# Kernel tuning notes

Measured on AMD Instinct MI355X. Metric: run time of the kernel, lower is better.

## Reference

```python
import jax, jax.numpy as jnp
import numpy as np

NEG_SLOPE = 0.2
BN_EPS = 1e-5


def gat_conv(x, src, dst, num_nodes, W, att_src, att_dst, bias, concat):
    # x: [N, F_in]; W: [F_in, H*C]; att_src/att_dst: [H, C]
    H, C = att_src.shape
    h = (x @ W).reshape(num_nodes, H, C)                 # [N, H, C]
    a_src = jnp.einsum('nhc,hc->nh', h, att_src)          # [N, H]
    a_dst = jnp.einsum('nhc,hc->nh', h, att_dst)          # [N, H]
    e = a_src[src] + a_dst[dst]                           # [E, H]
    e = jax.nn.leaky_relu(e, NEG_SLOPE)
    # segment softmax over edges sharing the same destination node
    m = jax.ops.segment_max(e, dst, num_segments=num_nodes)   # [N, H]
    ex = jnp.exp(e - m[dst])
    denom = jax.ops.segment_sum(ex, dst, num_segments=num_nodes)  # [N, H]
    alpha = ex / (denom[dst] + 1e-16)                     # [E, H]
    msg = h[src] * alpha[:, :, None]                      # [E, H, C]
    out = jax.ops.segment_sum(msg, dst, num_segments=num_nodes)   # [N, H, C]
    if concat:
        return out.reshape(num_nodes, H * C) + bias
    return out.mean(axis=1) + bias


def batch_norm(x, gamma, beta):
    mu = x.mean(axis=0)
    var = x.var(axis=0)
    return (x - mu) * jax.lax.rsqrt(var + BN_EPS) * gamma + beta


def setup_inputs() -> dict:
    key = jax.random.key(0)
    ks = jax.random.split(key, 16)
    N, E, F_in, C, H, NC = 50000, 800000, 128, 16, 8, 2
    s = lambda k, shape, fan: jax.random.normal(k, shape, jnp.float32) * (1.0 / np.sqrt(fan))
    inp = {
        'x': jax.random.normal(ks[0], (N, F_in), jnp.float32),
        'edge_index': jax.random.randint(ks[1], (2, E), 0, N, jnp.int32),
        'W0': s(ks[2], (F_in, H * C), F_in),
        'att_src0': s(ks[3], (H, C), C),
        'att_dst0': s(ks[4], (H, C), C),
        'b0': jnp.zeros((H * C,), jnp.float32),
        'gamma0': jnp.ones((H * C,), jnp.float32),
        'beta0': jnp.zeros((H * C,), jnp.float32),
        'W1': s(ks[5], (H * C, H * C), H * C),
        'att_src1': s(ks[6], (H, C), C),
        'att_dst1': s(ks[7], (H, C), C),
        'b1': jnp.zeros((C,), jnp.float32),
        'gamma1': jnp.ones((C,), jnp.float32),
        'beta1': jnp.zeros((C,), jnp.float32),
        'Wc': s(ks[8], (C, NC), C),
        'bc': jnp.zeros((NC,), jnp.float32),
    }
    return inp


def reference(x, edge_index, W0, att_src0, att_dst0, b0, gamma0, beta0,
              W1, att_src1, att_dst1, b1, gamma1, beta1, Wc, bc):
    N = x.shape[0]
    loop = jnp.arange(N, dtype=edge_index.dtype)
    src = jnp.concatenate([edge_index[0], loop])  # add self-loops (PyG default)
    dst = jnp.concatenate([edge_index[1], loop])
    # layer 0: concat heads -> [N, H*C]
    h = gat_conv(x, src, dst, N, W0, att_src0, att_dst0, b0, concat=True)
    h = batch_norm(h, gamma0, beta0)
    h = jax.nn.elu(h)
    # layer 1: average heads -> [N, C]
    h = gat_conv(h, src, dst, N, W1, att_src1, att_dst1, b1, concat=False)
    h = batch_norm(h, gamma1, beta1)
    logits = h @ Wc + bc
    return logits
```

## Files before the change

kernel.cpp:

```cpp
#include <hip/hip_runtime.h>
#include <math.h>

#define NEG_SLOPE 0.2f
#define BN_EPS 1e-5f


__device__ __forceinline__ void edge_sd(const int* __restrict__ ei, int E, int eid, int& s, int& d) {
    if (eid < E) { s = ei[eid]; d = ei[E + eid]; }
    else         { s = d = eid - E; }
}

__device__ __forceinline__ float lrelu(float v) { return v > 0.f ? v : NEG_SLOPE * v; }

__device__ __forceinline__ unsigned short f2bf(float f) {
    unsigned u = __float_as_uint(f);
    u += 0x7fffu + ((u >> 16) & 1u);
    return (unsigned short)(u >> 16);
}

__global__ __launch_bounds__(256) void gemm128(const float* __restrict__ X,
                                               const float* __restrict__ W,
                                               float* __restrict__ Y,
                                               unsigned short* __restrict__ Ybf,
                                               const float* __restrict__ bnmu,
                                               const float* __restrict__ bnrs,
                                               const float* __restrict__ gamma,
                                               const float* __restrict__ beta,
                                               int Nrows) {
    __shared__ float xs[64 * 128];
    int bm = blockIdx.x * 64;
    int tid = threadIdx.x;

    const float4* Xv = (const float4*)(X + (size_t)bm * 128);
    float4* xsv = (float4*)xs;
    if (bnmu == nullptr) {
        for (int i = tid; i < 64 * 32; i += 256) {
            int row = i >> 5;
            xsv[i] = (bm + row < Nrows) ? Xv[i] : make_float4(0.f, 0.f, 0.f, 0.f);
        }
    } else {
        for (int i = tid; i < 64 * 32; i += 256) {
            int row = i >> 5;
            int cb = (i & 31) * 4;
            float4 v = (bm + row < Nrows) ? Xv[i] : make_float4(0.f, 0.f, 0.f, 0.f);
            float4 m4 = *(const float4*)(bnmu + cb);
            float4 r4 = *(const float4*)(bnrs + cb);
            float4 g4 = *(const float4*)(gamma + cb);
            float4 b4 = *(const float4*)(beta + cb);
            v.x = (v.x - m4.x) * r4.x * g4.x + b4.x;
            v.y = (v.y - m4.y) * r4.y * g4.y + b4.y;
            v.z = (v.z - m4.z) * r4.z * g4.z + b4.z;
            v.w = (v.w - m4.w) * r4.w * g4.w + b4.w;
            v.x = v.x > 0.f ? v.x : expm1f(v.x);
            v.y = v.y > 0.f ? v.y : expm1f(v.y);
            v.z = v.z > 0.f ? v.z : expm1f(v.z);
            v.w = v.w > 0.f ? v.w : expm1f(v.w);
            xsv[i] = v;
        }
    }
    __syncthreads();

    int cq = tid & 31;
    int rg = tid >> 5;

    float acc[8][4];
#pragma unroll
    for (int r = 0; r < 8; r++)
#pragma unroll
        for (int j = 0; j < 4; j++) acc[r][j] = 0.f;

    const float* xbase = xs + (rg * 8) * 128;
#pragma unroll 4
    for (int k = 0; k < 128; k++) {
        float4 w4 = *(const float4*)(W + k * 128 + cq * 4);
#pragma unroll
        for (int r = 0; r < 8; r++) {
            float xv = xbase[r * 128 + k];
            acc[r][0] += xv * w4.x;
            acc[r][1] += xv * w4.y;
            acc[r][2] += xv * w4.z;
            acc[r][3] += xv * w4.w;
        }
    }
#pragma unroll
    for (int r = 0; r < 8; r++) {
        int row = bm + rg * 8 + r;
        if (row < Nrows) {
            *(float4*)(Y + (size_t)row * 128 + cq * 4) =
                make_float4(acc[r][0], acc[r][1], acc[r][2], acc[r][3]);
            ushort4 pk;
            pk.x = f2bf(acc[r][0]);
            pk.y = f2bf(acc[r][1]);
            pk.z = f2bf(acc[r][2]);
            pk.w = f2bf(acc[r][3]);
            *(ushort4*)(Ybf + (size_t)row * 128 + cq * 4) = pk;
        }
    }
}

__global__ void att_kernel(const float* __restrict__ Hm,
                           const float* __restrict__ att_s,
                           const float* __restrict__ att_d,
                           float* __restrict__ a_src, float* __restrict__ a_dst, int N) {
    int idx = blockIdx.x * 256 + threadIdx.x;
    if (idx >= N * 8) return;
    int n = idx >> 3, h = idx & 7;
    const float* hp = Hm + (size_t)n * 128 + h * 16;
    float ss = 0.f, sd = 0.f;
#pragma unroll
    for (int c = 0; c < 16; c++) {
        float v = hp[c];
        ss += v * att_s[h * 16 + c];
        sd += v * att_d[h * 16 + c];
    }
    a_src[idx] = ss;
    a_dst[idx] = sd;
}

__global__ void hist_kernel(const int* __restrict__ ei, int E, int Etot,
                            int* __restrict__ counts, int* __restrict__ rank) {
    int eid = blockIdx.x * 256 + threadIdx.x;
    if (eid >= Etot) return;
    int s, d;
    edge_sd(ei, E, eid, s, d);
    rank[eid] = atomicAdd(&counts[d], 1);
}

__global__ __launch_bounds__(256) void chunksum_kernel(const int* __restrict__ counts,
                                                       int* __restrict__ csum, int N) {
    __shared__ int red[256];
    int base = blockIdx.x * 1024;
    int s = 0;
    for (int i = threadIdx.x; i < 1024; i += 256) {
        int idx = base + i;
        s += (idx < N) ? counts[idx] : 0;
    }
    red[threadIdx.x] = s;
    __syncthreads();
#pragma unroll
    for (int st = 128; st > 0; st >>= 1) {
        if (threadIdx.x < st) red[threadIdx.x] += red[threadIdx.x + st];
        __syncthreads();
    }
    if (threadIdx.x == 0) csum[blockIdx.x] = red[0];
}

__global__ void chunkscan_kernel(int* __restrict__ csum, int nchunk) {
    int lane = threadIdx.x;
    int v = (lane < nchunk) ? csum[lane] : 0;
    int incl = v;
#pragma unroll
    for (int off = 1; off < 64; off <<= 1) {
        int t = __shfl_up(incl, off);
        if (lane >= off) incl += t;
    }
    if (lane < nchunk) csum[lane] = incl - v;
}

__global__ __launch_bounds__(1024) void scanfinal_kernel(const int* __restrict__ counts,
                                                         const int* __restrict__ csum,
                                                         int* __restrict__ rowptr, int N) {
    __shared__ int wsum[16], woff_s[16];
    int tid = threadIdx.x, lane = tid & 63, wid = tid >> 6;
    int idx = blockIdx.x * 1024 + tid;
    int v = (idx < N) ? counts[idx] : 0;
    int incl = v;
#pragma unroll
    for (int off = 1; off < 64; off <<= 1) {
        int t = __shfl_up(incl, off);
        if (lane >= off) incl += t;
    }
    if (lane == 63) wsum[wid] = incl;
    __syncthreads();
    if (wid == 0 && lane < 16) {
        int w = wsum[lane], iw = w;
#pragma unroll
        for (int off = 1; off < 16; off <<= 1) {
            int t = __shfl_up(iw, off);
            if (lane >= off) iw += t;
        }
        woff_s[lane] = iw - w;
    }
    __syncthreads();
    if (idx < N) rowptr[idx + 1] = csum[blockIdx.x] + woff_s[wid] + incl;
    if (blockIdx.x == 0 && tid == 0) rowptr[0] = 0;
}

__global__ void scatter_kernel(const int* __restrict__ ei, int E, int Etot,
                               const int* __restrict__ rowptr, const int* __restrict__ rank,
                               unsigned short* __restrict__ ssrc) {
    int eid = blockIdx.x * 256 + threadIdx.x;
    if (eid >= Etot) return;
    int s, d;
    edge_sd(ei, E, eid, s, d);
    ssrc[rowptr[d] + rank[eid]] = (unsigned short)s;
}

template <bool MEAN>
__global__ __launch_bounds__(256) void agg_kernel(const int* __restrict__ rowptr,
                                                  const unsigned short* __restrict__ ssrc,
                                                  const float* __restrict__ a_src,
                                                  const float* __restrict__ a_dst,
                                                  const unsigned short* __restrict__ Hbf,
                                                  float* __restrict__ outbuf, int N) {
    int wid = threadIdx.x >> 6;
    int dst = blockIdx.x * 4 + wid;
    if (dst >= N) return;
    int lane = threadIdx.x & 63;
    int j  = lane >> 3;
    int hj = lane & 7;
    int hf = lane >> 3;
    int f  = lane * 2;
    int start = rowptr[dst], end = rowptr[dst + 1];
    float adst = a_dst[dst * 8 + hj];

    float acc0 = 0.f, acc1 = 0.f, denl = 0.f;
    for (int base = start; base < end; base += 8) {
        int i = base + j;
        int s = (i < end) ? (int)ssrc[i] : -1;
        float w = 0.f;
        if (s >= 0) w = __expf(lrelu(a_src[s * 8 + hj] + adst));
        denl += w;

        int   sA[8];
        float wA[8];
        unsigned uA[8];
#pragma unroll
        for (int j2 = 0; j2 < 8; j2++) {
            sA[j2] = __shfl(s, j2 * 8);
            wA[j2] = __shfl(w, j2 * 8 + hf);
        }
#pragma unroll
        for (int j2 = 0; j2 < 8; j2++)
            uA[j2] = (sA[j2] >= 0) ? *(const unsigned*)(Hbf + (size_t)sA[j2] * 128 + f) : 0u;
#pragma unroll
        for (int j2 = 0; j2 < 8; j2++) {
            acc0 += wA[j2] * __uint_as_float(uA[j2] << 16);
            acc1 += wA[j2] * __uint_as_float(uA[j2] & 0xffff0000u);
        }
    }
#pragma unroll
    for (int off = 8; off < 64; off <<= 1) denl += __shfl_xor(denl, off);
    float den = __shfl(denl, hf);
    float inv = 1.f / (den + 1e-16f);
    if (!MEAN) {
        *(float2*)(outbuf + (size_t)dst * 128 + f) = make_float2(acc0 * inv, acc1 * inv);
    } else {
        float r0 = acc0 * inv, r1 = acc1 * inv;
#pragma unroll
        for (int off = 8; off < 64; off <<= 1) {
            r0 += __shfl_xor(r0, off);
            r1 += __shfl_xor(r1, off);
        }
        if (lane < 8)
            *(float2*)(outbuf + (size_t)dst * 16 + lane * 2) =
                make_float2(r0 * 0.125f, r1 * 0.125f);
    }
}

template <int C>
__global__ __launch_bounds__(256) void stats_part_kernel(const float* __restrict__ X, int Nrows,
                                                         float* __restrict__ partial,
                                                         int rows_per_block) {
    constexpr int GSZ = 256 / C;
    __shared__ float ls[256], lq[256];
    int c = threadIdx.x % C;
    int g = threadIdx.x / C;
    long base = (long)blockIdx.x * rows_per_block;
    long endr = base + rows_per_block;
    if (endr > Nrows) endr = Nrows;
    float s = 0.f, q = 0.f;
    for (long r = base + g; r < endr; r += GSZ) {
        float v = X[r * C + c];
        s += v;
        q += v * v;
    }
    ls[threadIdx.x] = s;
    lq[threadIdx.x] = q;
    __syncthreads();
#pragma unroll
    for (int st = GSZ / 2; st > 0; st >>= 1) {
        if (g < st) {
            ls[threadIdx.x] += ls[threadIdx.x + st * C];
            lq[threadIdx.x] += lq[threadIdx.x + st * C];
        }
        __syncthreads();
    }
    if (g == 0) {
        partial[(size_t)blockIdx.x * (2 * C) + c] = ls[c];
        partial[(size_t)blockIdx.x * (2 * C) + C + c] = lq[c];
    }
}

template <int C>
__global__ __launch_bounds__(1024) void stats_final_kernel(const float* __restrict__ partial,
                                                           int nblk, float invN,
                                                           float* __restrict__ mu,
                                                           float* __restrict__ rsig) {
    constexpr int G = 1024 / C;
    __shared__ float ls[1024], lq[1024];
    int c = threadIdx.x % C;
    int g = threadIdx.x / C;
    float s = 0.f, q = 0.f;
    for (int b = g; b < nblk; b += G) {
        s += partial[(size_t)b * (2 * C) + c];
        q += partial[(size_t)b * (2 * C) + C + c];
    }
    ls[threadIdx.x] = s;
    lq[threadIdx.x] = q;
    __syncthreads();
#pragma unroll
    for (int st = G / 2; st > 0; st >>= 1) {
        if (g < st) {
            ls[threadIdx.x] += ls[threadIdx.x + st * C];
            lq[threadIdx.x] += lq[threadIdx.x + st * C];
        }
        __syncthreads();
    }
    if (g == 0) {
        float m_ = ls[c] * invN;
        float v = lq[c] * invN - m_ * m_;
        mu[c] = m_;
        rsig[c] = rsqrtf(v + BN_EPS);
    }
}

__global__ void final_kernel(const float* __restrict__ out1,
                             const float* __restrict__ mu, const float* __restrict__ rsig,
                             const float* __restrict__ gamma, const float* __restrict__ beta,
                             const float* __restrict__ Wc, const float* __restrict__ bc,
                             float* __restrict__ out, int N) {
    int n = blockIdx.x * 256 + threadIdx.x;
    if (n >= N) return;
    float l0 = bc[0], l1 = bc[1];
#pragma unroll
    for (int c = 0; c < 16; c++) {
        float v = (out1[(size_t)n * 16 + c] - mu[c]) * rsig[c] * gamma[c] + beta[c];
        l0 += v * Wc[c * 2 + 0];
        l1 += v * Wc[c * 2 + 1];
    }
    out[(size_t)n * 2 + 0] = l0;
    out[(size_t)n * 2 + 1] = l1;
}

extern "C" void kernel_launch(void* const* d_in, const int* in_sizes, int n_in,
                              void* d_out, int out_size, void* d_ws, size_t ws_size,
                              hipStream_t stream) {
    const float* x   = (const float*)d_in[0];
    const int*   ei  = (const int*)d_in[1];
    const float* W0  = (const float*)d_in[2];
    const float* as0 = (const float*)d_in[3];
    const float* ad0 = (const float*)d_in[4];
    const float* g0  = (const float*)d_in[6];
    const float* be0 = (const float*)d_in[7];
    const float* W1  = (const float*)d_in[8];
    const float* as1 = (const float*)d_in[9];
    const float* ad1 = (const float*)d_in[10];
    const float* g1  = (const float*)d_in[12];
    const float* be1 = (const float*)d_in[13];
    const float* Wc  = (const float*)d_in[14];
    const float* bc  = (const float*)d_in[15];
    float* out = (float*)d_out;

    int N = in_sizes[0] / 128;
    int E = in_sizes[1] / 2;
    int Etot = E + N;

    char* ws = (char*)d_ws;
    size_t off = 0;
    auto walloc = [&](size_t bytes) -> void* {
        void* p = ws + off;
        off += (bytes + 255) & ~(size_t)255;
        return p;
    };
    float*          A       = (float*)walloc((size_t)N * 128 * 4);
    float*          B       = (float*)walloc((size_t)N * 128 * 4);
    unsigned short* Hbf     = (unsigned short*)walloc((size_t)N * 128 * 2);
    float*          a_src   = (float*)walloc((size_t)N * 8 * 4);
    float*          a_dst   = (float*)walloc((size_t)N * 8 * 4);
    float*          out1    = (float*)walloc((size_t)N * 16 * 4);
    int*            counts  = (int*)walloc((size_t)N * 4);
    int*            rowptr  = (int*)walloc((size_t)(N + 1) * 4);
    int*            rank    = (int*)walloc((size_t)Etot * 4);
    int*            csum    = (int*)walloc(64 * 4);
    unsigned short* ssrc    = (unsigned short*)walloc((size_t)Etot * 2);
    float*          partial = (float*)walloc((size_t)256 * 256 * 4);
    float*          stats   = (float*)walloc(2 * 128 * 4);
    float* mu = stats, * rsig = stats + 128;

    dim3 b256(256);
    int gN64    = (N + 63) / 64;
    int gNH     = (N * 8 + 255) / 256;
    int gE      = (Etot + 255) / 256;
    int gAgg    = (N + 3) / 4;
    int nchunk  = (N + 1023) / 1024;
    const int SBLK = 256;
    int rpb = (N + SBLK - 1) / SBLK;

    hipMemsetAsync(counts, 0, (size_t)N * 4, stream);
    hist_kernel<<<gE, b256, 0, stream>>>(ei, E, Etot, counts, rank);
    chunksum_kernel<<<nchunk, b256, 0, stream>>>(counts, csum, N);
    chunkscan_kernel<<<1, 64, 0, stream>>>(csum, nchunk);
    scanfinal_kernel<<<nchunk, 1024, 0, stream>>>(counts, csum, rowptr, N);
    scatter_kernel<<<gE, b256, 0, stream>>>(ei, E, Etot, rowptr, rank, ssrc);

    gemm128<<<gN64, b256, 0, stream>>>(x, W0, A, Hbf, nullptr, nullptr, nullptr, nullptr, N);
    att_kernel<<<gNH, b256, 0, stream>>>(A, as0, ad0, a_src, a_dst, N);
    agg_kernel<false><<<gAgg, b256, 0, stream>>>(rowptr, ssrc, a_src, a_dst, Hbf, B, N);
    stats_part_kernel<128><<<SBLK, b256, 0, stream>>>(B, N, partial, rpb);
    stats_final_kernel<128><<<1, 1024, 0, stream>>>(partial, SBLK, 1.0f / N, mu, rsig);

    gemm128<<<gN64, b256, 0, stream>>>(B, W1, B, Hbf, mu, rsig, g0, be0, N);
    att_kernel<<<gNH, b256, 0, stream>>>(B, as1, ad1, a_src, a_dst, N);
    agg_kernel<true><<<gAgg, b256, 0, stream>>>(rowptr, ssrc, a_src, a_dst, Hbf, out1, N);
    stats_part_kernel<16><<<SBLK, b256, 0, stream>>>(out1, N, partial, rpb);
    stats_final_kernel<16><<<1, 1024, 0, stream>>>(partial, SBLK, 1.0f / N, mu, rsig);
    final_kernel<<<(N + 255) / 256, b256, 0, stream>>>(out1, mu, rsig, g1, be1, Wc, bc, out, N);
}
```

Measured before the change: 357.4 us.

## Fuse attention logits into GEMM epilogue and prefetch edges in aggregation

Computes per-head a_src/a_dst dot products inside the GEMM epilogue with lane shuffles, which removes the separate att_kernel and the fp32 H write and re-read. The GEMM inner loop now reads four k values per step using float4 shared-memory loads. The aggregation loop software-prefetches the next group's source index and a_src value so their latency overlaps the feature gathers. The cost is higher register pressure in both kernels.

```diff
diff --git a/kernel.cpp b/kernel.cpp
--- a/kernel.cpp
+++ b/kernel.cpp
@@ -20,8 +20,11 @@
 
 __global__ __launch_bounds__(256) void gemm128(const float* __restrict__ X,
                                                const float* __restrict__ W,
-                                               float* __restrict__ Y,
                                                unsigned short* __restrict__ Ybf,
+                                               const float* __restrict__ att_s,
+                                               const float* __restrict__ att_d,
+                                               float* __restrict__ a_srcO,
+                                               float* __restrict__ a_dstO,
                                                const float* __restrict__ bnmu,
                                                const float* __restrict__ bnrs,
                                                const float* __restrict__ gamma,
@@ -62,6 +65,7 @@
 
     int cq = tid & 31;
     int rg = tid >> 5;
+    int lane = tid & 63;
 
     float acc[8][4];
 #pragma unroll
@@ -70,51 +74,51 @@
         for (int j = 0; j < 4; j++) acc[r][j] = 0.f;
 
     const float* xbase = xs + (rg * 8) * 128;
-#pragma unroll 4
-    for (int k = 0; k < 128; k++) {
-        float4 w4 = *(const float4*)(W + k * 128 + cq * 4);
+#pragma unroll 2
+    for (int k4 = 0; k4 < 32; k4++) {
+        const float* wrow = W + k4 * 4 * 128 + cq * 4;
+        float4 w0 = *(const float4*)(wrow);
+        float4 w1 = *(const float4*)(wrow + 128);
+        float4 w2 = *(const float4*)(wrow + 256);
+        float4 w3 = *(const float4*)(wrow + 384);
 #pragma unroll
         for (int r = 0; r < 8; r++) {
-            float xv = xbase[r * 128 + k];
-            acc[r][0] += xv * w4.x;
-            acc[r][1] += xv * w4.y;
-            acc[r][2] += xv * w4.z;
-            acc[r][3] += xv * w4.w;
-        }
-    }
+            float4 x4 = *(const float4*)(xbase + r * 128 + k4 * 4);
+            acc[r][0] += x4.x * w0.x; acc[r][1] += x4.x * w0.y;
+            acc[r][2] += x4.x * w0.z; acc[r][3] += x4.x * w0.w;
+            acc[r][0] += x4.y * w1.x; acc[r][1] += x4.y * w1.y;
+            acc[r][2] += x4.y * w1.z; acc[r][3] += x4.y * w1.w;
+            acc[r][0] += x4.z * w2.x; acc[r][1] += x4.z * w2.y;
+            acc[r][2] += x4.z * w2.z; acc[r][3] += x4.z * w2.w;
+            acc[r][0] += x4.w * w3.x; acc[r][1] += x4.w * w3.y;
+            acc[r][2] += x4.w * w3.z; acc[r][3] += x4.w * w3.w;
+        }
+    }
+
+    int h = cq >> 2;
+    float4 as4 = *(const float4*)(att_s + h * 16 + (cq & 3) * 4);
+    float4 ad4 = *(const float4*)(att_d + h * 16 + (cq & 3) * 4);
+
 #pragma unroll
     for (int r = 0; r < 8; r++) {
         int row = bm + rg * 8 + r;
+        float ps = acc[r][0] * as4.x + acc[r][1] * as4.y + acc[r][2] * as4.z + acc[r][3] * as4.w;
+        float pd = acc[r][0] * ad4.x + acc[r][1] * ad4.y + acc[r][2] * ad4.z + acc[r][3] * ad4.w;
+        ps += __shfl_xor(ps, 1); ps += __shfl_xor(ps, 2);
+        pd += __shfl_xor(pd, 1); pd += __shfl_xor(pd, 2);
         if (row < Nrows) {
-            *(float4*)(Y + (size_t)row * 128 + cq * 4) =
-                make_float4(acc[r][0], acc[r][1], acc[r][2], acc[r][3]);
             ushort4 pk;
             pk.x = f2bf(acc[r][0]);
             pk.y = f2bf(acc[r][1]);
             pk.z = f2bf(acc[r][2]);
             pk.w = f2bf(acc[r][3]);
             *(ushort4*)(Ybf + (size_t)row * 128 + cq * 4) = pk;
-        }
-    }
-}
-
-__global__ void att_kernel(const float* __restrict__ Hm,
-                           const float* __restrict__ att_s,
-                           const float* __restrict__ att_d,
-                           float* __restrict__ a_src, float* __restrict__ a_dst, int N) {
-    int idx = blockIdx.x * 256 + threadIdx.x;
-    if (idx >= N * 8) return;
-    int n = idx >> 3, h = idx & 7;
-    const float* hp = Hm + (size_t)n * 128 + h * 16;
-    float ss = 0.f, sd = 0.f;
-#pragma unroll
-    for (int c = 0; c < 16; c++) {
-        float v = hp[c];
-        ss += v * att_s[h * 16 + c];
-        sd += v * att_d[h * 16 + c];
-    }
-    a_src[idx] = ss;
-    a_dst[idx] = sd;
+            if ((lane & 3) == 0) {
+                a_srcO[row * 8 + h] = ps;
+                a_dstO[row * 8 + h] = pd;
+            }
+        }
+    }
 }
 
 __global__ void hist_kernel(const int* __restrict__ ei, int E, int Etot,
@@ -215,29 +219,37 @@
     float adst = a_dst[dst * 8 + hj];
 
     float acc0 = 0.f, acc1 = 0.f, denl = 0.f;
+
+    int i = start + j;
+    int s = (i < end) ? (int)ssrc[i] : -1;
+    float ar = (s >= 0) ? a_src[s * 8 + hj] : 0.f;
+
     for (int base = start; base < end; base += 8) {
-        int i = base + j;
-        int s = (i < end) ? (int)ssrc[i] : -1;
-        float w = 0.f;
-        if (s >= 0) w = __expf(lrelu(a_src[s * 8 + hj] + adst));
-        denl += w;
-
-        int   sA[8];
-        float wA[8];
+        int sA[8];
+#pragma unroll
+        for (int j2 = 0; j2 < 8; j2++) sA[j2] = __shfl(s, j2 * 8);
         unsigned uA[8];
-#pragma unroll
-        for (int j2 = 0; j2 < 8; j2++) {
-            sA[j2] = __shfl(s, j2 * 8);
-            wA[j2] = __shfl(w, j2 * 8 + hf);
-        }
 #pragma unroll
         for (int j2 = 0; j2 < 8; j2++)
             uA[j2] = (sA[j2] >= 0) ? *(const unsigned*)(Hbf + (size_t)sA[j2] * 128 + f) : 0u;
+
+        int inext = base + 8 + j;
+        int snext = (inext < end) ? (int)ssrc[inext] : -1;
+        float anext = (snext >= 0) ? a_src[snext * 8 + hj] : 0.f;
+
+        float w = (s >= 0) ? __expf(lrelu(ar + adst)) : 0.f;
+        denl += w;
+        float wA[8];
+#pragma unroll
+        for (int j2 = 0; j2 < 8; j2++) wA[j2] = __shfl(w, j2 * 8 + hf);
+
 #pragma unroll
         for (int j2 = 0; j2 < 8; j2++) {
             acc0 += wA[j2] * __uint_as_float(uA[j2] << 16);
             acc1 += wA[j2] * __uint_as_float(uA[j2] & 0xffff0000u);
         }
+        s = snext;
+        ar = anext;
     }
 #pragma unroll
     for (int off = 8; off < 64; off <<= 1) denl += __shfl_xor(denl, off);
@@ -373,7 +385,6 @@
         off += (bytes + 255) & ~(size_t)255;
         return p;
     };
-    float*          A       = (float*)walloc((size_t)N * 128 * 4);
     float*          B       = (float*)walloc((size_t)N * 128 * 4);
     unsigned short* Hbf     = (unsigned short*)walloc((size_t)N * 128 * 2);
     float*          a_src   = (float*)walloc((size_t)N * 8 * 4);
@@ -390,7 +401,6 @@
 
     dim3 b256(256);
     int gN64    = (N + 63) / 64;
-    int gNH     = (N * 8 + 255) / 256;
     int gE      = (Etot + 255) / 256;
     int gAgg    = (N + 3) / 4;
     int nchunk  = (N + 1023) / 1024;
@@ -404,14 +414,14 @@
     scanfinal_kernel<<<nchunk, 1024, 0, stream>>>(counts, csum, rowptr, N);
     scatter_kernel<<<gE, b256, 0, stream>>>(ei, E, Etot, rowptr, rank, ssrc);
 
-    gemm128<<<gN64, b256, 0, stream>>>(x, W0, A, Hbf, nullptr, nullptr, nullptr, nullptr, N);
-    att_kernel<<<gNH, b256, 0, stream>>>(A, as0, ad0, a_src, a_dst, N);
+    gemm128<<<gN64, b256, 0, stream>>>(x, W0, Hbf, as0, ad0, a_src, a_dst,
+                                       nullptr, nullptr, nullptr, nullptr, N);
     agg_kernel<false><<<gAgg, b256, 0, stream>>>(rowptr, ssrc, a_src, a_dst, Hbf, B, N);
     stats_part_kernel<128><<<SBLK, b256, 0, stream>>>(B, N, partial, rpb);
     stats_final_kernel<128><<<1, 1024, 0, stream>>>(partial, SBLK, 1.0f / N, mu, rsig);
 
-    gemm128<<<gN64, b256, 0, stream>>>(B, W1, B, Hbf, mu, rsig, g0, be0, N);
-    att_kernel<<<gNH, b256, 0, stream>>>(B, as1, ad1, a_src, a_dst, N);
+    gemm128<<<gN64, b256, 0, stream>>>(B, W1, Hbf, as1, ad1, a_src, a_dst,
+                                       mu, rsig, g0, be0, N);
     agg_kernel<true><<<gAgg, b256, 0, stream>>>(rowptr, ssrc, a_src, a_dst, Hbf, out1, N);
     stats_part_kernel<16><<<SBLK, b256, 0, stream>>>(out1, N, partial, rpb);
     stats_final_kernel<16><<<1, 1024, 0, stream>>>(partial, SBLK, 1.0f / N, mu, rsig);
```

Result: faster. 346.8 us (-3.0%).
